# Kernel tuning notes

Hardware: AMD Instinct MI355X
Metric: run time of the kernel (lower is better)

The kernel has to match this reference:

```python
import jax, jax.numpy as jnp
import numpy as np

HIDDEN = 2048
INTER = 1408
NUM_EXPERTS = 8
TOP_K = 2
BATCH, SEQ = 2, 1024


def setup_inputs() -> dict:
    key = jax.random.key(0)
    ks = jax.random.split(key, 8)
    s = 0.02
    return {
        "x": jax.random.normal(ks[0], (BATCH, SEQ, HIDDEN), dtype=jnp.float32),
        "router_w": jax.random.normal(ks[1], (NUM_EXPERTS, HIDDEN), dtype=jnp.float32) * s,
        "gate_w": jax.random.normal(ks[2], (NUM_EXPERTS, INTER, HIDDEN), dtype=jnp.float32) * s,
        "up_w": jax.random.normal(ks[3], (NUM_EXPERTS, INTER, HIDDEN), dtype=jnp.float32) * s,
        "down_w": jax.random.normal(ks[4], (NUM_EXPERTS, HIDDEN, INTER), dtype=jnp.float32) * s,
        "shared_gate_w": jax.random.normal(ks[5], (INTER, HIDDEN), dtype=jnp.float32) * s,
        "shared_up_w": jax.random.normal(ks[6], (INTER, HIDDEN), dtype=jnp.float32) * s,
        "shared_down_w": jax.random.normal(ks[7], (HIDDEN, INTER), dtype=jnp.float32) * s,
    }


def reference(x, router_w, gate_w, up_w, down_w,
              shared_gate_w, shared_up_w, shared_down_w):
    B, S, H = x.shape
    T = B * S
    E = router_w.shape[0]
    xf = x.reshape(T, H)

    # Router: softmax over experts, top-k selection, renormalized weights
    logits = xf @ router_w.T                       # [T, E]
    probs = jax.nn.softmax(logits, axis=-1)
    topw, topi = jax.lax.top_k(probs, TOP_K)       # [T, K]
    topw = topw / jnp.sum(topw, axis=-1, keepdims=True)

    # Combine weight per (token, expert): scatter-add of top-k weights
    comb = jnp.zeros((T, E), dtype=xf.dtype).at[
        jnp.arange(T)[:, None], topi].add(topw)    # [T, E]

    # All-expert SwiGLU (grouped GEMM form of masked gather/MLP/scatter)
    g = jnp.einsum('th,eih->tei', xf, gate_w)      # [T, E, I]
    u = jnp.einsum('th,eih->tei', xf, up_w)
    hmid = jax.nn.silu(g) * u
    eo = jnp.einsum('tei,ehi->teh', hmid, down_w)  # [T, E, H]
    out = jnp.einsum('te,teh->th', comb, eo)       # weighted combine

    # Shared expert applied to every token
    sh = (jax.nn.silu(xf @ shared_gate_w.T) * (xf @ shared_up_w.T)) @ shared_down_w.T
    out = out + sh
    return out.reshape(B, S, H)
```

## Files before the change

### kernel.cpp

```cpp
#include <hip/hip_runtime.h>
#include <cstdint>
#include <cstddef>

#define T_TOK 2048
#define HID   2048
#define INTER 1408
#define NEXP  8
#define NPAIR 6144
#define LDST  40

typedef __bf16 bf16x8 __attribute__((ext_vector_type(8)));
typedef float  floatx4 __attribute__((ext_vector_type(4)));

static const size_t XB_OFF   = 0;
static const size_t HM_OFF   = XB_OFF + (size_t)T_TOK * HID * 2;
static const size_t TOK_OFF  = HM_OFF + (size_t)NPAIR * INTER * 2;
static const size_t WGT_OFF  = TOK_OFF + (size_t)NPAIR * 4;
static const size_t TE_OFF   = WGT_OFF + (size_t)NPAIR * 4;
static const size_t TW_OFF   = TE_OFF + (size_t)T_TOK * 2 * 4;
static const size_t CTRL_OFF = TW_OFF + (size_t)T_TOK * 2 * 4;

static __device__ __forceinline__ unsigned short f2bf(float f) {
    unsigned u = __float_as_uint(f);
    u += 0x7fffu + ((u >> 16) & 1u);
    return (unsigned short)(u >> 16);
}
static __device__ __forceinline__ unsigned pk2(float a, float b) {
    return (unsigned)f2bf(a) | ((unsigned)f2bf(b) << 16);
}

__global__ __launch_bounds__(256) void k_cvt_x(const float* __restrict__ x,
                                               unsigned short* __restrict__ xb) {
    int gid = blockIdx.x * 256 + threadIdx.x;
    const float4* src = (const float4*)x;
    float4 a = src[gid * 2], b = src[gid * 2 + 1];
    uint4 o;
    o.x = pk2(a.x, a.y); o.y = pk2(a.z, a.w);
    o.z = pk2(b.x, b.y); o.w = pk2(b.z, b.w);
    ((uint4*)xb)[gid] = o;
}

__global__ __launch_bounds__(256) void k_router(const float* __restrict__ x,
                                                const float* __restrict__ rw,
                                                int* __restrict__ te, float* __restrict__ tw,
                                                int* __restrict__ counts) {
    int wave = threadIdx.x >> 6, lane = threadIdx.x & 63;
    int t = blockIdx.x * 4 + wave;
    const float* xp = x + (size_t)t * HID;

    float acc[8];
#pragma unroll
    for (int e = 0; e < 8; ++e) acc[e] = 0.f;
    for (int i = lane; i < HID; i += 64) {
        float xv = xp[i];
#pragma unroll
        for (int e = 0; e < 8; ++e) acc[e] = fmaf(xv, rw[e * HID + i], acc[e]);
    }
#pragma unroll
    for (int e = 0; e < 8; ++e) {
        float v = acc[e];
        for (int s = 32; s; s >>= 1) v += __shfl_xor(v, s, 64);
        acc[e] = v;
    }
    float mx = acc[0];
#pragma unroll
    for (int e = 1; e < 8; ++e) mx = fmaxf(mx, acc[e]);
    float p[8];
#pragma unroll
    for (int e = 0; e < 8; ++e) p[e] = __expf(acc[e] - mx);
    int i1 = 0; float v1 = p[0];
#pragma unroll
    for (int e = 1; e < 8; ++e) if (p[e] > v1) { v1 = p[e]; i1 = e; }
    int i2 = -1; float v2 = -1.f;
#pragma unroll
    for (int e = 0; e < 8; ++e) if (e != i1 && p[e] > v2) { v2 = p[e]; i2 = e; }
    float inv = 1.f / (v1 + v2);
    if (lane == 0) {
        te[2 * t] = i1;     tw[2 * t] = v1 * inv;
        te[2 * t + 1] = i2; tw[2 * t + 1] = v2 * inv;
        atomicAdd(&counts[i1], 1);
        atomicAdd(&counts[i2], 1);
    }
}

__global__ void k_offsets(int* __restrict__ ctrl) {
    if (threadIdx.x == 0) {
        int s = 0;
        for (int e = 0; e < 8; ++e) { ctrl[16 + e] = s; s += ctrl[e]; }
        ctrl[16 + 8] = s;
        ctrl[8] = T_TOK;
    }
}

__global__ __launch_bounds__(256) void k_scatter(const int* __restrict__ te,
                                                 const float* __restrict__ tw,
                                                 const int* __restrict__ offsets,
                                                 int* __restrict__ fill,
                                                 int* __restrict__ tok, float* __restrict__ wgt) {
    int t = blockIdx.x * 256 + threadIdx.x;
    if (t >= T_TOK) return;
#pragma unroll
    for (int k = 0; k < 2; ++k) {
        int e = te[2 * t + k];
        int slot = atomicAdd(&fill[e], 1);
        int pp = offsets[e] + slot;
        tok[pp] = t; wgt[pp] = tw[2 * t + k];
    }
    tok[2 * T_TOK + t] = t; wgt[2 * T_TOK + t] = 1.0f;
}

__global__ __launch_bounds__(256) void k_gemm1(const unsigned short* __restrict__ xb,
                                               const float* __restrict__ gate_w,
                                               const float* __restrict__ up_w,
                                               const float* __restrict__ sgate,
                                               const float* __restrict__ sup,
                                               const int* __restrict__ tok,
                                               const int* __restrict__ ctrl,
                                               unsigned short* __restrict__ hmid) {
    int e = blockIdx.z;
    int cnt = ctrl[e];
    int m0 = blockIdx.y * 128;
    if (m0 >= cnt) return;
    int off = ctrl[16 + e];
    int i0 = blockIdx.x * 64;
    const float* gw = (e < 8) ? gate_w + (size_t)e * INTER * HID : sgate;
    const float* uw = (e < 8) ? up_w + (size_t)e * INTER * HID : sup;

    __shared__ __align__(16) unsigned short As[128 * LDST];
    __shared__ __align__(16) unsigned short Bg[64 * LDST];
    __shared__ __align__(16) unsigned short Bu[64 * LDST];

    int tid = threadIdx.x;
    int lane = tid & 63, wave = tid >> 6;
    int ar = tid >> 1, ac = (tid & 1) * 16;
    int ap = off + m0 + ar; if (ap > NPAIR - 1) ap = NPAIR - 1;
    const unsigned short* asrc = xb + (size_t)tok[ap] * HID + ac;
    int br = tid >> 2, bc = (tid & 3) * 8;
    const float* gsrc = gw + (size_t)(i0 + br) * HID + bc;
    const float* usrc = uw + (size_t)(i0 + br) * HID + bc;

    floatx4 accg[2][4], accu[2][4];
#pragma unroll
    for (int mi = 0; mi < 2; ++mi)
#pragma unroll
        for (int ni = 0; ni < 4; ++ni) {
            accg[mi][ni] = (floatx4){0.f, 0.f, 0.f, 0.f};
            accu[mi][ni] = (floatx4){0.f, 0.f, 0.f, 0.f};
        }

    int wm = wave * 32;
    int mrow = lane & 15, kq = (lane >> 4) * 8;

    for (int kt = 0; kt < HID / 32; ++kt) {
        int h0 = kt * 32;
        uint4 av0 = *(const uint4*)(asrc + h0);
        uint4 av1 = *(const uint4*)(asrc + h0 + 8);
        float4 g0 = *(const float4*)(gsrc + h0);
        float4 g1 = *(const float4*)(gsrc + h0 + 4);
        float4 u0 = *(const float4*)(usrc + h0);
        float4 u1 = *(const float4*)(usrc + h0 + 4);
        __syncthreads();
        *(uint4*)&As[ar * LDST + ac] = av0;
        *(uint4*)&As[ar * LDST + ac + 8] = av1;
        uint4 bg; bg.x = pk2(g0.x, g0.y); bg.y = pk2(g0.z, g0.w);
        bg.z = pk2(g1.x, g1.y); bg.w = pk2(g1.z, g1.w);
        *(uint4*)&Bg[br * LDST + bc] = bg;
        uint4 bu; bu.x = pk2(u0.x, u0.y); bu.y = pk2(u0.z, u0.w);
        bu.z = pk2(u1.x, u1.y); bu.w = pk2(u1.z, u1.w);
        *(uint4*)&Bu[br * LDST + bc] = bu;
        __syncthreads();

        bf16x8 af[2];
#pragma unroll
        for (int mi = 0; mi < 2; ++mi)
            af[mi] = *(const bf16x8*)&As[(wm + mi * 16 + mrow) * LDST + kq];
#pragma unroll
        for (int ni = 0; ni < 4; ++ni) {
            bf16x8 bgv = *(const bf16x8*)&Bg[(ni * 16 + mrow) * LDST + kq];
            bf16x8 buv = *(const bf16x8*)&Bu[(ni * 16 + mrow) * LDST + kq];
#pragma unroll
            for (int mi = 0; mi < 2; ++mi) {
                accg[mi][ni] = __builtin_amdgcn_mfma_f32_16x16x32_bf16(af[mi], bgv, accg[mi][ni], 0, 0, 0);
                accu[mi][ni] = __builtin_amdgcn_mfma_f32_16x16x32_bf16(af[mi], buv, accu[mi][ni], 0, 0, 0);
            }
        }
    }

    int quad = lane >> 4, col = lane & 15;
#pragma unroll
    for (int mi = 0; mi < 2; ++mi)
#pragma unroll
        for (int ni = 0; ni < 4; ++ni)
#pragma unroll
            for (int r = 0; r < 4; ++r) {
                int row = m0 + wm + mi * 16 + quad * 4 + r;
                if (row < cnt) {
                    float g = accg[mi][ni][r], u = accu[mi][ni][r];
                    float s = g / (1.f + __expf(-g));
                    hmid[(size_t)(off + row) * INTER + i0 + ni * 16 + col] = f2bf(s * u);
                }
            }
}

__global__ __launch_bounds__(256) void k_gemm2(const unsigned short* __restrict__ hmid,
                                               const float* __restrict__ down_w,
                                               const float* __restrict__ sdown,
                                               const int* __restrict__ tok,
                                               const float* __restrict__ wgt,
                                               const int* __restrict__ ctrl,
                                               float* __restrict__ out) {
    int e = blockIdx.z;
    int cnt = ctrl[e];
    int m0 = blockIdx.y * 128;
    if (m0 >= cnt) return;
    int off = ctrl[16 + e];
    int n0 = blockIdx.x * 64;
    const float* dw = (e < 8) ? down_w + (size_t)e * HID * INTER : sdown;

    __shared__ __align__(16) unsigned short As[128 * LDST];
    __shared__ __align__(16) unsigned short Bd[64 * LDST];

    int tid = threadIdx.x;
    int lane = tid & 63, wave = tid >> 6;
    int ar = tid >> 1, ac = (tid & 1) * 16;
    int ap = off + m0 + ar; if (ap > NPAIR - 1) ap = NPAIR - 1;
    const unsigned short* asrc = hmid + (size_t)ap * INTER + ac;
    int br = tid >> 2, bc = (tid & 3) * 8;
    const float* bsrc = dw + (size_t)(n0 + br) * INTER + bc;

    floatx4 acc[2][4];
#pragma unroll
    for (int mi = 0; mi < 2; ++mi)
#pragma unroll
        for (int ni = 0; ni < 4; ++ni) acc[mi][ni] = (floatx4){0.f, 0.f, 0.f, 0.f};

    int wm = wave * 32;
    int mrow = lane & 15, kq = (lane >> 4) * 8;

    for (int kt = 0; kt < INTER / 32; ++kt) {
        int k0 = kt * 32;
        uint4 av0 = *(const uint4*)(asrc + k0);
        uint4 av1 = *(const uint4*)(asrc + k0 + 8);
        float4 b0 = *(const float4*)(bsrc + k0);
        float4 b1 = *(const float4*)(bsrc + k0 + 4);
        __syncthreads();
        *(uint4*)&As[ar * LDST + ac] = av0;
        *(uint4*)&As[ar * LDST + ac + 8] = av1;
        uint4 bd; bd.x = pk2(b0.x, b0.y); bd.y = pk2(b0.z, b0.w);
        bd.z = pk2(b1.x, b1.y); bd.w = pk2(b1.z, b1.w);
        *(uint4*)&Bd[br * LDST + bc] = bd;
        __syncthreads();

        bf16x8 af[2];
#pragma unroll
        for (int mi = 0; mi < 2; ++mi)
            af[mi] = *(const bf16x8*)&As[(wm + mi * 16 + mrow) * LDST + kq];
#pragma unroll
        for (int ni = 0; ni < 4; ++ni) {
            bf16x8 bv = *(const bf16x8*)&Bd[(ni * 16 + mrow) * LDST + kq];
#pragma unroll
            for (int mi = 0; mi < 2; ++mi)
                acc[mi][ni] = __builtin_amdgcn_mfma_f32_16x16x32_bf16(af[mi], bv, acc[mi][ni], 0, 0, 0);
        }
    }

    int quad = lane >> 4, col = lane & 15;
#pragma unroll
    for (int mi = 0; mi < 2; ++mi)
#pragma unroll
        for (int r = 0; r < 4; ++r) {
            int row = m0 + wm + mi * 16 + quad * 4 + r;
            if (row < cnt) {
                int p = off + row;
                int t = tok[p];
                float w = wgt[p];
#pragma unroll
                for (int ni = 0; ni < 4; ++ni)
                    atomicAdd(&out[(size_t)t * HID + n0 + ni * 16 + col], w * acc[mi][ni][r]);
            }
        }
}

extern "C" void kernel_launch(void* const* d_in, const int* in_sizes, int n_in,
                              void* d_out, int out_size, void* d_ws, size_t ws_size,
                              hipStream_t stream) {
    const float* x        = (const float*)d_in[0];
    const float* router_w = (const float*)d_in[1];
    const float* gate_w   = (const float*)d_in[2];
    const float* up_w     = (const float*)d_in[3];
    const float* down_w   = (const float*)d_in[4];
    const float* sgate    = (const float*)d_in[5];
    const float* sup      = (const float*)d_in[6];
    const float* sdown    = (const float*)d_in[7];
    float* out = (float*)d_out;

    char* ws = (char*)d_ws;
    unsigned short* xb   = (unsigned short*)(ws + XB_OFF);
    unsigned short* hmid = (unsigned short*)(ws + HM_OFF);
    int*   tok  = (int*)(ws + TOK_OFF);
    float* wgt  = (float*)(ws + WGT_OFF);
    int*   te   = (int*)(ws + TE_OFF);
    float* tw   = (float*)(ws + TW_OFF);
    int*   ctrl = (int*)(ws + CTRL_OFF);

    hipMemsetAsync(ctrl, 0, 48 * sizeof(int), stream);
    hipMemsetAsync(out, 0, (size_t)T_TOK * HID * sizeof(float), stream);

    k_cvt_x  <<<(T_TOK * HID) / 8 / 256, 256, 0, stream>>>(x, xb);
    k_router <<<T_TOK / 4, 256, 0, stream>>>(x, router_w, te, tw, ctrl);
    k_offsets<<<1, 64, 0, stream>>>(ctrl);
    k_scatter<<<T_TOK / 256, 256, 0, stream>>>(te, tw, ctrl + 16, ctrl + 32, tok, wgt);

    k_gemm1<<<dim3(INTER / 64, 16, 9), 256, 0, stream>>>(xb, gate_w, up_w, sgate, sup, tok, ctrl, hmid);
    k_gemm2<<<dim3(HID / 64, 16, 9), 256, 0, stream>>>(hmid, down_w, sdown, tok, wgt, ctrl, out);
}
```

Before: 628.9 us.

## Pre-convert expert weights to bf16 and stream GEMM tiles directly into LDS

Adds a kernel that converts all expert and shared-expert weights from fp32 to bf16 workspace buffers on every call. Both grouped GEMMs then load A and B tiles with global_load_lds straight into shared memory, with no register staging or in-loop fp32-to-bf16 packing. The goal is to halve weight bytes per tile load and cut VALU and register pressure in the main loop. In exchange, each call pays a full extra pass over all weights, the LDS row padding is dropped (possible bank conflicts), and loads are still not double-buffered.

```diff
diff --git a/kernel.cpp b/kernel.cpp
--- a/kernel.cpp
+++ b/kernel.cpp
@@ -7,14 +7,18 @@
 #define INTER 1408
 #define NEXP  8
 #define NPAIR 6144
-#define LDST  40
+#define SLICE 2883584
+#define BKS   32
 
 typedef __bf16 bf16x8 __attribute__((ext_vector_type(8)));
 typedef float  floatx4 __attribute__((ext_vector_type(4)));
 
 static const size_t XB_OFF   = 0;
 static const size_t HM_OFF   = XB_OFF + (size_t)T_TOK * HID * 2;
-static const size_t TOK_OFF  = HM_OFF + (size_t)NPAIR * INTER * 2;
+static const size_t GB_OFF   = HM_OFF + (size_t)NPAIR * INTER * 2;
+static const size_t UB_OFF   = GB_OFF + (size_t)9 * SLICE * 2;
+static const size_t DB_OFF   = UB_OFF + (size_t)9 * SLICE * 2;
+static const size_t TOK_OFF  = DB_OFF + (size_t)9 * SLICE * 2;
 static const size_t WGT_OFF  = TOK_OFF + (size_t)NPAIR * 4;
 static const size_t TE_OFF   = WGT_OFF + (size_t)NPAIR * 4;
 static const size_t TW_OFF   = TE_OFF + (size_t)T_TOK * 2 * 4;
@@ -27,6 +31,11 @@
 }
 static __device__ __forceinline__ unsigned pk2(float a, float b) {
     return (unsigned)f2bf(a) | ((unsigned)f2bf(b) << 16);
+}
+static __device__ __forceinline__ void g2l16(const void* g, void* l) {
+    __builtin_amdgcn_global_load_lds(
+        (const __attribute__((address_space(1))) unsigned int*)g,
+        (__attribute__((address_space(3))) unsigned int*)l, 16, 0, 0);
 }
 
 __global__ __launch_bounds__(256) void k_cvt_x(const float* __restrict__ x,
@@ -40,6 +49,37 @@
     ((uint4*)xb)[gid] = o;
 }
 
+__global__ __launch_bounds__(256) void k_cvt_w(const float* __restrict__ g,
+                                               const float* __restrict__ u,
+                                               const float* __restrict__ d,
+                                               const float* __restrict__ sg,
+                                               const float* __restrict__ su,
+                                               const float* __restrict__ sd,
+                                               unsigned short* __restrict__ gb,
+                                               unsigned short* __restrict__ ub,
+                                               unsigned short* __restrict__ db) {
+    int sl = blockIdx.z;
+    const float* src;
+    unsigned short* dst;
+    if (blockIdx.y == 0) {
+        src = (sl < 8) ? g + (size_t)sl * SLICE : sg;
+        dst = gb + (size_t)sl * SLICE;
+    } else if (blockIdx.y == 1) {
+        src = (sl < 8) ? u + (size_t)sl * SLICE : su;
+        dst = ub + (size_t)sl * SLICE;
+    } else {
+        src = (sl < 8) ? d + (size_t)sl * SLICE : sd;
+        dst = db + (size_t)sl * SLICE;
+    }
+    int gid = blockIdx.x * 256 + threadIdx.x;
+    const float4* s4 = (const float4*)src;
+    float4 a = s4[gid * 2], b = s4[gid * 2 + 1];
+    uint4 o;
+    o.x = pk2(a.x, a.y); o.y = pk2(a.z, a.w);
+    o.z = pk2(b.x, b.y); o.w = pk2(b.z, b.w);
+    ((uint4*)dst)[gid] = o;
+}
+
 __global__ __launch_bounds__(256) void k_router(const float* __restrict__ x,
                                                 const float* __restrict__ rw,
                                                 int* __restrict__ te, float* __restrict__ tw,
@@ -110,10 +150,8 @@
 }
 
 __global__ __launch_bounds__(256) void k_gemm1(const unsigned short* __restrict__ xb,
-                                               const float* __restrict__ gate_w,
-                                               const float* __restrict__ up_w,
-                                               const float* __restrict__ sgate,
-                                               const float* __restrict__ sup,
+                                               const unsigned short* __restrict__ gwb,
+                                               const unsigned short* __restrict__ uwb,
                                                const int* __restrict__ tok,
                                                const int* __restrict__ ctrl,
                                                unsigned short* __restrict__ hmid) {
@@ -123,21 +161,29 @@
     if (m0 >= cnt) return;
     int off = ctrl[16 + e];
     int i0 = blockIdx.x * 64;
-    const float* gw = (e < 8) ? gate_w + (size_t)e * INTER * HID : sgate;
-    const float* uw = (e < 8) ? up_w + (size_t)e * INTER * HID : sup;
-
-    __shared__ __align__(16) unsigned short As[128 * LDST];
-    __shared__ __align__(16) unsigned short Bg[64 * LDST];
-    __shared__ __align__(16) unsigned short Bu[64 * LDST];
+    const unsigned short* gw = gwb + (size_t)e * SLICE;
+    const unsigned short* uw = uwb + (size_t)e * SLICE;
+
+    __shared__ __align__(16) unsigned short As[128 * BKS];
+    __shared__ __align__(16) unsigned short Bg[64 * BKS];
+    __shared__ __align__(16) unsigned short Bu[64 * BKS];
 
     int tid = threadIdx.x;
     int lane = tid & 63, wave = tid >> 6;
-    int ar = tid >> 1, ac = (tid & 1) * 16;
-    int ap = off + m0 + ar; if (ap > NPAIR - 1) ap = NPAIR - 1;
-    const unsigned short* asrc = xb + (size_t)tok[ap] * HID + ac;
-    int br = tid >> 2, bc = (tid & 3) * 8;
-    const float* gsrc = gw + (size_t)(i0 + br) * HID + bc;
-    const float* usrc = uw + (size_t)(i0 + br) * HID + bc;
+    int lr = lane >> 2, lc = (lane & 3) * 8;
+
+    int r0 = m0 + wave * 32 + lr;
+    int ap0 = off + r0;       if (ap0 > NPAIR - 1) ap0 = NPAIR - 1;
+    int ap1 = off + r0 + 16;  if (ap1 > NPAIR - 1) ap1 = NPAIR - 1;
+    const unsigned short* a0 = xb + (size_t)tok[ap0] * HID + lc;
+    const unsigned short* a1 = xb + (size_t)tok[ap1] * HID + lc;
+    const unsigned short* bg = gw + (size_t)(i0 + wave * 16 + lr) * HID + lc;
+    const unsigned short* bu = uw + (size_t)(i0 + wave * 16 + lr) * HID + lc;
+
+    unsigned short* lA0 = &As[(wave * 32) * BKS];
+    unsigned short* lA1 = &As[(wave * 32 + 16) * BKS];
+    unsigned short* lBg = &Bg[(wave * 16) * BKS];
+    unsigned short* lBu = &Bu[(wave * 16) * BKS];
 
     floatx4 accg[2][4], accu[2][4];
 #pragma unroll
@@ -151,39 +197,29 @@
     int wm = wave * 32;
     int mrow = lane & 15, kq = (lane >> 4) * 8;
 
-    for (int kt = 0; kt < HID / 32; ++kt) {
-        int h0 = kt * 32;
-        uint4 av0 = *(const uint4*)(asrc + h0);
-        uint4 av1 = *(const uint4*)(asrc + h0 + 8);
-        float4 g0 = *(const float4*)(gsrc + h0);
-        float4 g1 = *(const float4*)(gsrc + h0 + 4);
-        float4 u0 = *(const float4*)(usrc + h0);
-        float4 u1 = *(const float4*)(usrc + h0 + 4);
+    for (int kt = 0; kt < HID / BKS; ++kt) {
+        int k0 = kt * BKS;
+        g2l16(a0 + k0, lA0);
+        g2l16(a1 + k0, lA1);
+        g2l16(bg + k0, lBg);
+        g2l16(bu + k0, lBu);
         __syncthreads();
-        *(uint4*)&As[ar * LDST + ac] = av0;
-        *(uint4*)&As[ar * LDST + ac + 8] = av1;
-        uint4 bg; bg.x = pk2(g0.x, g0.y); bg.y = pk2(g0.z, g0.w);
-        bg.z = pk2(g1.x, g1.y); bg.w = pk2(g1.z, g1.w);
-        *(uint4*)&Bg[br * LDST + bc] = bg;
-        uint4 bu; bu.x = pk2(u0.x, u0.y); bu.y = pk2(u0.z, u0.w);
-        bu.z = pk2(u1.x, u1.y); bu.w = pk2(u1.z, u1.w);
-        *(uint4*)&Bu[br * LDST + bc] = bu;
-        __syncthreads();
 
         bf16x8 af[2];
 #pragma unroll
         for (int mi = 0; mi < 2; ++mi)
-            af[mi] = *(const bf16x8*)&As[(wm + mi * 16 + mrow) * LDST + kq];
+            af[mi] = *(const bf16x8*)&As[(wm + mi * 16 + mrow) * BKS + kq];
 #pragma unroll
         for (int ni = 0; ni < 4; ++ni) {
-            bf16x8 bgv = *(const bf16x8*)&Bg[(ni * 16 + mrow) * LDST + kq];
-            bf16x8 buv = *(const bf16x8*)&Bu[(ni * 16 + mrow) * LDST + kq];
+            bf16x8 bgv = *(const bf16x8*)&Bg[(ni * 16 + mrow) * BKS + kq];
+            bf16x8 buv = *(const bf16x8*)&Bu[(ni * 16 + mrow) * BKS + kq];
 #pragma unroll
             for (int mi = 0; mi < 2; ++mi) {
                 accg[mi][ni] = __builtin_amdgcn_mfma_f32_16x16x32_bf16(af[mi], bgv, accg[mi][ni], 0, 0, 0);
                 accu[mi][ni] = __builtin_amdgcn_mfma_f32_16x16x32_bf16(af[mi], buv, accu[mi][ni], 0, 0, 0);
             }
         }
+        __syncthreads();
     }
 
     int quad = lane >> 4, col = lane & 15;
@@ -203,8 +239,7 @@
 }
 
 __global__ __launch_bounds__(256) void k_gemm2(const unsigned short* __restrict__ hmid,
-                                               const float* __restrict__ down_w,
-                                               const float* __restrict__ sdown,
+                                               const unsigned short* __restrict__ dwb,
                                                const int* __restrict__ tok,
                                                const float* __restrict__ wgt,
                                                const int* __restrict__ ctrl,
@@ -215,18 +250,25 @@
     if (m0 >= cnt) return;
     int off = ctrl[16 + e];
     int n0 = blockIdx.x * 64;
-    const float* dw = (e < 8) ? down_w + (size_t)e * HID * INTER : sdown;
-
-    __shared__ __align__(16) unsigned short As[128 * LDST];
-    __shared__ __align__(16) unsigned short Bd[64 * LDST];
+    const unsigned short* dw = dwb + (size_t)e * SLICE;
+
+    __shared__ __align__(16) unsigned short As[128 * BKS];
+    __shared__ __align__(16) unsigned short Bd[64 * BKS];
 
     int tid = threadIdx.x;
     int lane = tid & 63, wave = tid >> 6;
-    int ar = tid >> 1, ac = (tid & 1) * 16;
-    int ap = off + m0 + ar; if (ap > NPAIR - 1) ap = NPAIR - 1;
-    const unsigned short* asrc = hmid + (size_t)ap * INTER + ac;
-    int br = tid >> 2, bc = (tid & 3) * 8;
-    const float* bsrc = dw + (size_t)(n0 + br) * INTER + bc;
+    int lr = lane >> 2, lc = (lane & 3) * 8;
+
+    int r0 = m0 + wave * 32 + lr;
+    int ap0 = off + r0;       if (ap0 > NPAIR - 1) ap0 = NPAIR - 1;
+    int ap1 = off + r0 + 16;  if (ap1 > NPAIR - 1) ap1 = NPAIR - 1;
+    const unsigned short* a0 = hmid + (size_t)ap0 * INTER + lc;
+    const unsigned short* a1 = hmid + (size_t)ap1 * INTER + lc;
+    const unsigned short* bd = dw + (size_t)(n0 + wave * 16 + lr) * INTER + lc;
+
+    unsigned short* lA0 = &As[(wave * 32) * BKS];
+    unsigned short* lA1 = &As[(wave * 32 + 16) * BKS];
+    unsigned short* lBd = &Bd[(wave * 16) * BKS];
 
     floatx4 acc[2][4];
 #pragma unroll
@@ -237,31 +279,25 @@
     int wm = wave * 32;
     int mrow = lane & 15, kq = (lane >> 4) * 8;
 
-    for (int kt = 0; kt < INTER / 32; ++kt) {
-        int k0 = kt * 32;
-        uint4 av0 = *(const uint4*)(asrc + k0);
-        uint4 av1 = *(const uint4*)(asrc + k0 + 8);
-        float4 b0 = *(const float4*)(bsrc + k0);
-        float4 b1 = *(const float4*)(bsrc + k0 + 4);
+    for (int kt = 0; kt < INTER / BKS; ++kt) {
+        int k0 = kt * BKS;
+        g2l16(a0 + k0, lA0);
+        g2l16(a1 + k0, lA1);
+        g2l16(bd + k0, lBd);
         __syncthreads();
-        *(uint4*)&As[ar * LDST + ac] = av0;
-        *(uint4*)&As[ar * LDST + ac + 8] = av1;
-        uint4 bd; bd.x = pk2(b0.x, b0.y); bd.y = pk2(b0.z, b0.w);
-        bd.z = pk2(b1.x, b1.y); bd.w = pk2(b1.z, b1.w);
-        *(uint4*)&Bd[br * LDST + bc] = bd;
-        __syncthreads();
 
         bf16x8 af[2];
 #pragma unroll
         for (int mi = 0; mi < 2; ++mi)
-            af[mi] = *(const bf16x8*)&As[(wm + mi * 16 + mrow) * LDST + kq];
+            af[mi] = *(const bf16x8*)&As[(wm + mi * 16 + mrow) * BKS + kq];
 #pragma unroll
         for (int ni = 0; ni < 4; ++ni) {
-            bf16x8 bv = *(const bf16x8*)&Bd[(ni * 16 + mrow) * LDST + kq];
+            bf16x8 bv = *(const bf16x8*)&Bd[(ni * 16 + mrow) * BKS + kq];
 #pragma unroll
             for (int mi = 0; mi < 2; ++mi)
                 acc[mi][ni] = __builtin_amdgcn_mfma_f32_16x16x32_bf16(af[mi], bv, acc[mi][ni], 0, 0, 0);
         }
+        __syncthreads();
     }
 
     int quad = lane >> 4, col = lane & 15;
@@ -297,6 +333,9 @@
     char* ws = (char*)d_ws;
     unsigned short* xb   = (unsigned short*)(ws + XB_OFF);
     unsigned short* hmid = (unsigned short*)(ws + HM_OFF);
+    unsigned short* gwb  = (unsigned short*)(ws + GB_OFF);
+    unsigned short* uwb  = (unsigned short*)(ws + UB_OFF);
+    unsigned short* dwb  = (unsigned short*)(ws + DB_OFF);
     int*   tok  = (int*)(ws + TOK_OFF);
     float* wgt  = (float*)(ws + WGT_OFF);
     int*   te   = (int*)(ws + TE_OFF);
@@ -307,10 +346,12 @@
     hipMemsetAsync(out, 0, (size_t)T_TOK * HID * sizeof(float), stream);
 
     k_cvt_x  <<<(T_TOK * HID) / 8 / 256, 256, 0, stream>>>(x, xb);
+    k_cvt_w  <<<dim3(SLICE / 8 / 256, 3, 9), 256, 0, stream>>>(gate_w, up_w, down_w,
+                                                               sgate, sup, sdown, gwb, uwb, dwb);
     k_router <<<T_TOK / 4, 256, 0, stream>>>(x, router_w, te, tw, ctrl);
     k_offsets<<<1, 64, 0, stream>>>(ctrl);
     k_scatter<<<T_TOK / 256, 256, 0, stream>>>(te, tw, ctrl + 16, ctrl + 32, tok, wgt);
 
-    k_gemm1<<<dim3(INTER / 64, 16, 9), 256, 0, stream>>>(xb, gate_w, up_w, sgate, sup, tok, ctrl, hmid);
-    k_gemm2<<<dim3(HID / 64, 16, 9), 256, 0, stream>>>(hmid, down_w, sdown, tok, wgt, ctrl, out);
-}
+    k_gemm1<<<dim3(INTER / 64, 16, 9), 256, 0, stream>>>(xb, gwb, uwb, tok, ctrl, hmid);
+    k_gemm2<<<dim3(HID / 64, 16, 9), 256, 0, stream>>>(hmid, dwb, tok, wgt, ctrl, out);
+}
```

New measurement: 620.3 us. About the same (-1.4%).
